# Kernel optimization log

Measured on AMD Instinct MI355X. Metric: run time of the kernel, lower is better.

The kernel has to match this reference:

```python
import jax, jax.numpy as jnp
import numpy as np

B, S, D, H = 4, 2048, 1024, 16
DH = D // H  # 64


def setup_inputs() -> dict:
    key = jax.random.key(0)
    ks = jax.random.split(key, 7)
    scale = 1.0 / np.sqrt(DH)
    return {
        "sequences": jax.random.normal(ks[0], (B, S, D), dtype=jnp.float32),
        # torch Linear weights: [out, in] per head -> stacked [H, DH, DH]
        "Wq": jax.random.uniform(ks[1], (H, DH, DH), jnp.float32, -scale, scale),
        "bq": jax.random.uniform(ks[2], (H, DH), jnp.float32, -scale, scale),
        "Wk": jax.random.uniform(ks[3], (H, DH, DH), jnp.float32, -scale, scale),
        "bk": jax.random.uniform(ks[4], (H, DH), jnp.float32, -scale, scale),
        "Wv": jax.random.uniform(ks[5], (H, DH, DH), jnp.float32, -scale, scale),
        "bv": jax.random.uniform(ks[6], (H, DH), jnp.float32, -scale, scale),
    }


def reference(sequences, Wq, bq, Wk, bk, Wv, bv):
    # split d into heads: [B, S, H, DH]
    x = sequences.reshape(B, S, H, DH)
    # per-head Linear: y = x @ W.T + b
    q = jnp.einsum("bshd,hed->bshe", x, Wq) + bq
    k = jnp.einsum("bshd,hed->bshe", x, Wk) + bk
    v = jnp.einsum("bshd,hed->bshe", x, Wv) + bv
    # scaled dot-product attention per head
    scores = jnp.einsum("bshd,bthd->bhst", q, k) / jnp.sqrt(jnp.float32(DH))
    attn = jax.nn.softmax(scores, axis=-1)
    out = jnp.einsum("bhst,bthd->bshd", attn, v)
    # hstack heads back to [B, S, D]
    return out.reshape(B, S, D)
```

## Files before the change

### kernel.cpp

```cpp
#include <hip/hip_runtime.h>
#include <hip/hip_bf16.h>


typedef unsigned short u16;
typedef unsigned int   u32;
typedef float  f32x4  __attribute__((ext_vector_type(4)));
typedef __bf16 bf16x4 __attribute__((ext_vector_type(4)));
typedef __bf16 bf16x8 __attribute__((ext_vector_type(8)));

#define NB 4
#define SS 2048
#define DDIM 1024
#define NH 16
#define DH 64

static __device__ __forceinline__ float fexp2(float x) {
#if __has_builtin(__builtin_amdgcn_exp2f)
    return __builtin_amdgcn_exp2f(x);
#else
    return exp2f(x);
#endif
}
static __device__ __forceinline__ bf16x4 cvt4(f32x4 v) {
    return __builtin_convertvector(v, bf16x4);
}

__global__ __launch_bounds__(256) void convert_w(
        const float* __restrict__ Wq, const float* __restrict__ Wk,
        const float* __restrict__ Wv, u16* __restrict__ Wb) {
    const int n4 = NH * DH * DH / 4;
    int i = blockIdx.x * 256 + threadIdx.x;
    int m = i / n4, r = i - m * n4;
    const float* src = (m == 0 ? Wq : (m == 1 ? Wk : Wv));
    f32x4 v = *(const f32x4*)(src + (size_t)r * 4);
    *(bf16x4*)((__bf16*)Wb + (size_t)m * NH * DH * DH + (size_t)r * 4) = cvt4(v);
}

__global__ __launch_bounds__(256) void qkv_kernel(
        const float* __restrict__ x, const u16* __restrict__ Wb,
        const float* __restrict__ bq, const float* __restrict__ bk,
        const float* __restrict__ bv,
        u16* __restrict__ Qw, u16* __restrict__ Kw, u16* __restrict__ Vt) {
    const int tid  = threadIdx.x;
    const int w    = tid >> 6;
    const int lane = tid & 63;
    const int quad = lane >> 4;
    const int c    = lane & 15;
    const int bid  = blockIdx.x;
    const int bh   = bid >> 5;
    const int s0   = (bid & 31) * 64;
    const int b    = bh >> 4, h = bh & 15;
    const int sb   = s0 + w * 16;

    const float* xr = x + ((size_t)(b * SS + sb + c)) * DDIM + h * DH;
    bf16x8 xb[2];
    #pragma unroll
    for (int kh = 0; kh < 2; ++kh) {
        f32x4 lo = *(const f32x4*)(xr + kh*32 + quad*8);
        f32x4 hi = *(const f32x4*)(xr + kh*32 + quad*8 + 4);
        bf16x4 a = cvt4(lo), bb = cvt4(hi);
        xb[kh] = __builtin_shufflevector(a, bb, 0, 1, 2, 3, 4, 5, 6, 7);
    }

    const int srow = sb + c;
    const size_t qkbase = (size_t)bh * SS * DH;
    const size_t vtbase = (size_t)bh * DH * SS;
    const int tq = srow & 31;
    const int sK = (srow & ~31) | ((tq & 4) << 2) | ((tq >> 3) << 2) | (tq & 3);

    #pragma unroll
    for (int m = 0; m < 2; ++m) {
        const __bf16* Wm = (const __bf16*)Wb + (size_t)m * NH * DH * DH + h * DH * DH;
        const float* bm = (m == 0 ? bq : bk) + h * DH;
        const float scale = (m == 0) ? 0.18033688f : 1.0f;
        const int drow = (m == 0) ? srow : sK;
        u16* base = (m == 0 ? Qw : Kw) + qkbase + (size_t)drow * DH;
        #pragma unroll
        for (int mt = 0; mt < 4; ++mt) {
            const __bf16* wr = Wm + (size_t)(mt*16 + c) * DH;
            bf16x8 a0 = *(const bf16x8*)(wr + quad*8);
            bf16x8 a1 = *(const bf16x8*)(wr + 32 + quad*8);
            f32x4 acc = {0.f, 0.f, 0.f, 0.f};
            acc = __builtin_amdgcn_mfma_f32_16x16x32_bf16(a0, xb[0], acc, 0, 0, 0);
            acc = __builtin_amdgcn_mfma_f32_16x16x32_bf16(a1, xb[1], acc, 0, 0, 0);
            f32x4 bias = *(const f32x4*)(bm + mt*16 + quad*4);
            f32x4 v = (acc + bias) * scale;
            *(bf16x4*)(base + mt*16 + quad*4) = cvt4(v);
        }
    }

    {
        const __bf16* Wm = (const __bf16*)Wb + (size_t)2 * NH * DH * DH + h * DH * DH;
        #pragma unroll
        for (int nt = 0; nt < 4; ++nt) {
            const __bf16* wr = Wm + (size_t)(nt*16 + c) * DH;
            bf16x8 b0 = *(const bf16x8*)(wr + quad*8);
            bf16x8 b1 = *(const bf16x8*)(wr + 32 + quad*8);
            f32x4 acc = {0.f, 0.f, 0.f, 0.f};
            acc = __builtin_amdgcn_mfma_f32_16x16x32_bf16(xb[0], b0, acc, 0, 0, 0);
            acc = __builtin_amdgcn_mfma_f32_16x16x32_bf16(xb[1], b1, acc, 0, 0, 0);
            const float bias = bv[h * DH + nt*16 + c];
            f32x4 v = acc + bias;
            u16* dst = Vt + vtbase + (size_t)(nt*16 + c) * SS + sb + quad*4;
            *(bf16x4*)dst = cvt4(v);
        }
    }
}

#define KT 64
#define KST 72
#define VST 72

__global__ __launch_bounds__(256, 2) void attn_kernel(
        const u16* __restrict__ Qw, const u16* __restrict__ Kw,
        const u16* __restrict__ Vt, float* __restrict__ out) {
    __shared__ __align__(16) u16 K_lds[KT * KST];
    __shared__ __align__(16) u16 V_lds[DH * VST];

    const int tid  = threadIdx.x;
    const int w    = tid >> 6;
    const int lane = tid & 63;
    const int quad = lane >> 4;
    const int c    = lane & 15;
    const int bid  = blockIdx.x;
    const int bh   = bid >> 3;
    const int q0   = (bid & 7) * 256;
    const int qw   = q0 + w * 64;

    const u16* Qb = Qw + (size_t)bh * SS * DH;
    const u16* Kb = Kw + (size_t)bh * SS * DH;
    const u16* Vb = Vt + (size_t)bh * DH * SS;

    bf16x8 qf[4][2];
    #pragma unroll
    for (int qt = 0; qt < 4; ++qt) {
        const u16* qrow = Qb + (size_t)(qw + qt*16 + c) * DH;
        qf[qt][0] = *(const bf16x8*)(qrow + quad*8);
        qf[qt][1] = *(const bf16x8*)(qrow + 32 + quad*8);
    }

    f32x4 o[4][4];
    f32x4 lacc[4];
    #pragma unroll
    for (int qt = 0; qt < 4; ++qt) {
        lacc[qt] = (f32x4){0.f, 0.f, 0.f, 0.f};
        #pragma unroll
        for (int dt = 0; dt < 4; ++dt) o[dt][qt] = (f32x4){0.f, 0.f, 0.f, 0.f};
    }

    bf16x8 ones8;
    { union { u16 u[8]; bf16x8 v; } one;
      #pragma unroll
      for (int i = 0; i < 8; ++i) one.u[i] = 0x3F80;
      ones8 = one.v; }

    const int strow = tid >> 2;
    const int stcol = (tid & 3) * 16;

    uint4 kr0 = *(const uint4*)(Kb + (size_t)strow * DH + stcol);
    uint4 kr1 = *(const uint4*)(Kb + (size_t)strow * DH + stcol + 8);
    uint4 vr0 = *(const uint4*)(Vb + (size_t)strow * SS + stcol);
    uint4 vr1 = *(const uint4*)(Vb + (size_t)strow * SS + stcol + 8);

    #pragma unroll 1
    for (int t0 = 0; t0 < SS; t0 += KT) {
        __syncthreads();
        *(uint4*)&K_lds[strow * KST + stcol]     = kr0;
        *(uint4*)&K_lds[strow * KST + stcol + 8] = kr1;
        *(uint4*)&V_lds[strow * VST + stcol]     = vr0;
        *(uint4*)&V_lds[strow * VST + stcol + 8] = vr1;
        __syncthreads();
        int tn = t0 + KT; if (tn >= SS) tn = 0;
        kr0 = *(const uint4*)(Kb + (size_t)(tn + strow) * DH + stcol);
        kr1 = *(const uint4*)(Kb + (size_t)(tn + strow) * DH + stcol + 8);
        vr0 = *(const uint4*)(Vb + (size_t)strow * SS + tn + stcol);
        vr1 = *(const uint4*)(Vb + (size_t)strow * SS + tn + stcol + 8);

        #pragma unroll
        for (int g = 0; g < 2; ++g) {
            bf16x8 kfA0 = *(const bf16x8*)&K_lds[(g*32 + c) * KST + quad*8];
            bf16x8 kfA1 = *(const bf16x8*)&K_lds[(g*32 + c) * KST + 32 + quad*8];
            bf16x8 kfB0 = *(const bf16x8*)&K_lds[(g*32 + 16 + c) * KST + quad*8];
            bf16x8 kfB1 = *(const bf16x8*)&K_lds[(g*32 + 16 + c) * KST + 32 + quad*8];
            bf16x8 vf[4];
            #pragma unroll
            for (int dt = 0; dt < 4; ++dt)
                vf[dt] = *(const bf16x8*)&V_lds[(dt*16 + c) * VST + g*32 + quad*8];

            #pragma unroll
            for (int qt = 0; qt < 4; ++qt) {
                f32x4 sA = {0.f,0.f,0.f,0.f}, sB = {0.f,0.f,0.f,0.f};
                sA = __builtin_amdgcn_mfma_f32_16x16x32_bf16(kfA0, qf[qt][0], sA, 0,0,0);
                sA = __builtin_amdgcn_mfma_f32_16x16x32_bf16(kfA1, qf[qt][1], sA, 0,0,0);
                sB = __builtin_amdgcn_mfma_f32_16x16x32_bf16(kfB0, qf[qt][0], sB, 0,0,0);
                sB = __builtin_amdgcn_mfma_f32_16x16x32_bf16(kfB1, qf[qt][1], sB, 0,0,0);
                f32x4 eA, eB;
                #pragma unroll
                for (int r = 0; r < 4; ++r) { eA[r] = fexp2(sA[r]); eB[r] = fexp2(sB[r]); }
                bf16x8 pf = __builtin_shufflevector(cvt4(eA), cvt4(eB), 0,1,2,3,4,5,6,7);
                #pragma unroll
                for (int dt = 0; dt < 4; ++dt)
                    o[dt][qt] = __builtin_amdgcn_mfma_f32_16x16x32_bf16(vf[dt], pf, o[dt][qt], 0,0,0);
                lacc[qt] = __builtin_amdgcn_mfma_f32_16x16x32_bf16(ones8, pf, lacc[qt], 0,0,0);
            }
        }
    }

    const int b = bh >> 4, h = bh & 15;
    #pragma unroll
    for (int qt = 0; qt < 4; ++qt) {
        const float inv = 1.0f / lacc[qt][0];
        const int token = qw + qt*16 + c;
        float* orow = out + ((size_t)b * SS + token) * DDIM + h * DH;
        #pragma unroll
        for (int dt = 0; dt < 4; ++dt) {
            f32x4 vv = o[dt][qt] * inv;
            *(f32x4*)(orow + dt*16 + quad*4) = vv;
        }
    }
}

extern "C" void kernel_launch(void* const* d_in, const int* in_sizes, int n_in,
                              void* d_out, int out_size, void* d_ws, size_t ws_size,
                              hipStream_t stream) {
    const float* x  = (const float*)d_in[0];
    const float* Wq = (const float*)d_in[1];
    const float* bq = (const float*)d_in[2];
    const float* Wk = (const float*)d_in[3];
    const float* bk = (const float*)d_in[4];
    const float* Wv = (const float*)d_in[5];
    const float* bv = (const float*)d_in[6];

    u16* Qw = (u16*)d_ws;
    u16* Kw = Qw + (size_t)NB * NH * SS * DH;
    u16* Vt = Kw + (size_t)NB * NH * SS * DH;
    u16* Wb = Vt + (size_t)NB * NH * SS * DH;

    convert_w<<<3 * NH * DH * DH / 4 / 256, 256, 0, stream>>>(Wq, Wk, Wv, Wb);
    qkv_kernel<<<NB * NH * (SS / 64), 256, 0, stream>>>(x, Wb, bq, bk, bv, Qw, Kw, Vt);
    attn_kernel<<<NB * NH * (SS / 256), 256, 0, stream>>>(Qw, Kw, Vt, (float*)d_out);
}
```

Before: 187.1 us.

## Fuse weight conversion into QKV kernel with LDS-staged weights and larger tiles

Drops the separate fp32-to-bf16 weight conversion kernel. The QKV kernel now converts the per-head weights itself into LDS and keeps them in registers, while each block covers 256 tokens instead of 64. Both kernels also reorder block indexing so consecutive blocks map to different batch-heads. This removes one launch and the repeated global weight reads, at the cost of more registers, an LDS staging step with a sync, and 512 QKV blocks instead of 2048.

```diff
diff --git a/kernel.cpp b/kernel.cpp
--- a/kernel.cpp
+++ b/kernel.cpp
@@ -24,83 +24,101 @@
 static __device__ __forceinline__ bf16x4 cvt4(f32x4 v) {
     return __builtin_convertvector(v, bf16x4);
 }
-
-__global__ __launch_bounds__(256) void convert_w(
-        const float* __restrict__ Wq, const float* __restrict__ Wk,
-        const float* __restrict__ Wv, u16* __restrict__ Wb) {
-    const int n4 = NH * DH * DH / 4;
-    int i = blockIdx.x * 256 + threadIdx.x;
-    int m = i / n4, r = i - m * n4;
-    const float* src = (m == 0 ? Wq : (m == 1 ? Wk : Wv));
-    f32x4 v = *(const f32x4*)(src + (size_t)r * 4);
-    *(bf16x4*)((__bf16*)Wb + (size_t)m * NH * DH * DH + (size_t)r * 4) = cvt4(v);
-}
+static __device__ __forceinline__ bf16x8 cvt8(f32x4 lo, f32x4 hi) {
+    return __builtin_shufflevector(cvt4(lo), cvt4(hi), 0, 1, 2, 3, 4, 5, 6, 7);
+}
+
+#define WST 72
 
 __global__ __launch_bounds__(256) void qkv_kernel(
-        const float* __restrict__ x, const u16* __restrict__ Wb,
-        const float* __restrict__ bq, const float* __restrict__ bk,
-        const float* __restrict__ bv,
+        const float* __restrict__ x,
+        const float* __restrict__ Wq, const float* __restrict__ bq,
+        const float* __restrict__ Wk, const float* __restrict__ bk,
+        const float* __restrict__ Wv, const float* __restrict__ bv,
         u16* __restrict__ Qw, u16* __restrict__ Kw, u16* __restrict__ Vt) {
+    __shared__ __align__(16) u16 W_lds[3 * DH * WST];
+
     const int tid  = threadIdx.x;
     const int w    = tid >> 6;
     const int lane = tid & 63;
     const int quad = lane >> 4;
     const int c    = lane & 15;
     const int bid  = blockIdx.x;
-    const int bh   = bid >> 5;
-    const int s0   = (bid & 31) * 64;
+    const int bh   = bid & 63;
+    const int s0   = (bid >> 6) * 256;
     const int b    = bh >> 4, h = bh & 15;
-    const int sb   = s0 + w * 16;
-
-    const float* xr = x + ((size_t)(b * SS + sb + c)) * DDIM + h * DH;
-    bf16x8 xb[2];
-    #pragma unroll
-    for (int kh = 0; kh < 2; ++kh) {
-        f32x4 lo = *(const f32x4*)(xr + kh*32 + quad*8);
-        f32x4 hi = *(const f32x4*)(xr + kh*32 + quad*8 + 4);
-        bf16x4 a = cvt4(lo), bb = cvt4(hi);
-        xb[kh] = __builtin_shufflevector(a, bb, 0, 1, 2, 3, 4, 5, 6, 7);
-    }
-
-    const int srow = sb + c;
+
+    {
+        const float* Wsrc[3] = {Wq + h*DH*DH, Wk + h*DH*DH, Wv + h*DH*DH};
+        #pragma unroll
+        for (int j = 0; j < 6; ++j) {
+            const int m = j >> 1;
+            const int chunk = ((j & 1) << 8) + tid;
+            const float* src = Wsrc[m] + chunk * 8;
+            f32x4 lo = *(const f32x4*)src;
+            f32x4 hi = *(const f32x4*)(src + 4);
+            const int row = chunk >> 3, c8 = chunk & 7;
+            *(bf16x8*)&W_lds[(m*DH + row) * WST + c8*8] = cvt8(lo, hi);
+        }
+    }
+    __syncthreads();
+
+    bf16x8 wf[3][4][2];
+    #pragma unroll
+    for (int m = 0; m < 3; ++m)
+        #pragma unroll
+        for (int mt = 0; mt < 4; ++mt)
+            #pragma unroll
+            for (int kh = 0; kh < 2; ++kh)
+                wf[m][mt][kh] = *(const bf16x8*)&W_lds[(m*DH + mt*16 + c) * WST + kh*32 + quad*8];
+
+    f32x4 biasQK[2][4];
+    float biasV[4];
+    #pragma unroll
+    for (int mt = 0; mt < 4; ++mt) {
+        biasQK[0][mt] = *(const f32x4*)(bq + h*DH + mt*16 + quad*4);
+        biasQK[1][mt] = *(const f32x4*)(bk + h*DH + mt*16 + quad*4);
+        biasV[mt] = bv[h*DH + mt*16 + c];
+    }
+
     const size_t qkbase = (size_t)bh * SS * DH;
     const size_t vtbase = (size_t)bh * DH * SS;
-    const int tq = srow & 31;
-    const int sK = (srow & ~31) | ((tq & 4) << 2) | ((tq >> 3) << 2) | (tq & 3);
-
-    #pragma unroll
-    for (int m = 0; m < 2; ++m) {
-        const __bf16* Wm = (const __bf16*)Wb + (size_t)m * NH * DH * DH + h * DH * DH;
-        const float* bm = (m == 0 ? bq : bk) + h * DH;
-        const float scale = (m == 0) ? 0.18033688f : 1.0f;
-        const int drow = (m == 0) ? srow : sK;
-        u16* base = (m == 0 ? Qw : Kw) + qkbase + (size_t)drow * DH;
-        #pragma unroll
-        for (int mt = 0; mt < 4; ++mt) {
-            const __bf16* wr = Wm + (size_t)(mt*16 + c) * DH;
-            bf16x8 a0 = *(const bf16x8*)(wr + quad*8);
-            bf16x8 a1 = *(const bf16x8*)(wr + 32 + quad*8);
+
+    #pragma unroll 1
+    for (int g = 0; g < 4; ++g) {
+        const int sb = s0 + w*64 + g*16;
+        const float* xr = x + ((size_t)(b * SS + sb + c)) * DDIM + h * DH;
+        bf16x8 xb[2];
+        #pragma unroll
+        for (int kh = 0; kh < 2; ++kh) {
+            f32x4 lo = *(const f32x4*)(xr + kh*32 + quad*8);
+            f32x4 hi = *(const f32x4*)(xr + kh*32 + quad*8 + 4);
+            xb[kh] = cvt8(lo, hi);
+        }
+
+        const int srow = sb + c;
+        const int tq = srow & 31;
+        const int sK = (srow & ~31) | ((tq & 4) << 2) | ((tq >> 3) << 2) | (tq & 3);
+
+        #pragma unroll
+        for (int m = 0; m < 2; ++m) {
+            const float scale = (m == 0) ? 0.18033688f : 1.0f;
+            u16* base = (m == 0 ? Qw : Kw) + qkbase + (size_t)(m == 0 ? srow : sK) * DH;
+            #pragma unroll
+            for (int mt = 0; mt < 4; ++mt) {
+                f32x4 acc = {0.f, 0.f, 0.f, 0.f};
+                acc = __builtin_amdgcn_mfma_f32_16x16x32_bf16(wf[m][mt][0], xb[0], acc, 0, 0, 0);
+                acc = __builtin_amdgcn_mfma_f32_16x16x32_bf16(wf[m][mt][1], xb[1], acc, 0, 0, 0);
+                f32x4 v = (acc + biasQK[m][mt]) * scale;
+                *(bf16x4*)(base + mt*16 + quad*4) = cvt4(v);
+            }
+        }
+        #pragma unroll
+        for (int nt = 0; nt < 4; ++nt) {
             f32x4 acc = {0.f, 0.f, 0.f, 0.f};
-            acc = __builtin_amdgcn_mfma_f32_16x16x32_bf16(a0, xb[0], acc, 0, 0, 0);
-            acc = __builtin_amdgcn_mfma_f32_16x16x32_bf16(a1, xb[1], acc, 0, 0, 0);
-            f32x4 bias = *(const f32x4*)(bm + mt*16 + quad*4);
-            f32x4 v = (acc + bias) * scale;
-            *(bf16x4*)(base + mt*16 + quad*4) = cvt4(v);
-        }
-    }
-
-    {
-        const __bf16* Wm = (const __bf16*)Wb + (size_t)2 * NH * DH * DH + h * DH * DH;
-        #pragma unroll
-        for (int nt = 0; nt < 4; ++nt) {
-            const __bf16* wr = Wm + (size_t)(nt*16 + c) * DH;
-            bf16x8 b0 = *(const bf16x8*)(wr + quad*8);
-            bf16x8 b1 = *(const bf16x8*)(wr + 32 + quad*8);
-            f32x4 acc = {0.f, 0.f, 0.f, 0.f};
-            acc = __builtin_amdgcn_mfma_f32_16x16x32_bf16(xb[0], b0, acc, 0, 0, 0);
-            acc = __builtin_amdgcn_mfma_f32_16x16x32_bf16(xb[1], b1, acc, 0, 0, 0);
-            const float bias = bv[h * DH + nt*16 + c];
-            f32x4 v = acc + bias;
+            acc = __builtin_amdgcn_mfma_f32_16x16x32_bf16(xb[0], wf[2][nt][0], acc, 0, 0, 0);
+            acc = __builtin_amdgcn_mfma_f32_16x16x32_bf16(xb[1], wf[2][nt][1], acc, 0, 0, 0);
+            f32x4 v = acc + biasV[nt];
             u16* dst = Vt + vtbase + (size_t)(nt*16 + c) * SS + sb + quad*4;
             *(bf16x4*)dst = cvt4(v);
         }
@@ -123,8 +141,8 @@
     const int quad = lane >> 4;
     const int c    = lane & 15;
     const int bid  = blockIdx.x;
-    const int bh   = bid >> 3;
-    const int q0   = (bid & 7) * 256;
+    const int bh   = bid & 63;
+    const int q0   = (bid >> 6) * 256;
     const int qw   = q0 + w * 64;
 
     const u16* Qb = Qw + (size_t)bh * SS * DH;
@@ -197,7 +215,7 @@
                 f32x4 eA, eB;
                 #pragma unroll
                 for (int r = 0; r < 4; ++r) { eA[r] = fexp2(sA[r]); eB[r] = fexp2(sB[r]); }
-                bf16x8 pf = __builtin_shufflevector(cvt4(eA), cvt4(eB), 0,1,2,3,4,5,6,7);
+                bf16x8 pf = cvt8(eA, eB);
                 #pragma unroll
                 for (int dt = 0; dt < 4; ++dt)
                     o[dt][qt] = __builtin_amdgcn_mfma_f32_16x16x32_bf16(vf[dt], pf, o[dt][qt], 0,0,0);
@@ -234,9 +252,8 @@
     u16* Qw = (u16*)d_ws;
     u16* Kw = Qw + (size_t)NB * NH * SS * DH;
     u16* Vt = Kw + (size_t)NB * NH * SS * DH;
-    u16* Wb = Vt + (size_t)NB * NH * SS * DH;
-
-    convert_w<<<3 * NH * DH * DH / 4 / 256, 256, 0, stream>>>(Wq, Wk, Wv, Wb);
-    qkv_kernel<<<NB * NH * (SS / 64), 256, 0, stream>>>(x, Wb, bq, bk, bv, Qw, Kw, Vt);
-    attn_kernel<<<NB * NH * (SS / 256), 256, 0, stream>>>(Qw, Kw, Vt, (float*)d_out);
-}
+
+    qkv_kernel<<<64 * (SS / 256), 256, 0, stream>>>(
+        x, Wq, bq, Wk, bk, Wv, bv, Qw, Kw, Vt);
+    attn_kernel<<<64 * (SS / 256), 256, 0, stream>>>(Qw, Kw, Vt, (float*)d_out);
+}
```

After: 179.8 us. 3.9% less time.
